# Performance work log

Measured on AMD Instinct MI355X. Metric: run time of the kernel, lower is better.

Reference implementation:

```python
import jax, jax.numpy as jnp
import numpy as np

B, T, N, F, H, K = 16, 24, 1329, 130, 15, 5


def setup_inputs() -> dict:
    key = jax.random.key(0)
    ks = jax.random.split(key, 14)
    var1 = 2.0 / (N + F)
    var2 = 2.0 / (F + 1)
    return {
        "seq": jax.random.uniform(ks[0], (B, T, N), jnp.float32),
        "A_hat": jax.random.uniform(ks[1], (N, N), jnp.float32) / N,  # normalized-adjacency scale
        "weight": jax.random.normal(ks[2], (N, F), jnp.float32) * var1,
        "bias": jax.random.normal(ks[3], (F,), jnp.float32) * var1,
        "weight2": jax.random.normal(ks[4], (F, 1), jnp.float32) * var2,
        "bias2": jax.random.normal(ks[5], (1,), jnp.float32) * var2,
        "W_ih": jax.random.normal(ks[6], (4 * H, N), jnp.float32) * 0.05,
        "W_hh": jax.random.normal(ks[7], (4 * H, H), jnp.float32) * 0.05,
        "b_ih": jax.random.normal(ks[8], (4 * H,), jnp.float32) * 0.05,
        "b_hh": jax.random.normal(ks[9], (4 * H,), jnp.float32) * 0.05,
        "h0": jax.random.normal(ks[10], (B, H), jnp.float32),
        "c0": jax.random.normal(ks[11], (B, H), jnp.float32),
        "fc_w": jax.random.normal(ks[12], (K, N, H), jnp.float32) * 0.05,
        "fc_b": jax.random.normal(ks[13], (K, N), jnp.float32) * 0.05,
    }


def reference(seq, A_hat, weight, bias, weight2, bias2,
              W_ih, W_hh, b_ih, b_hh, h0, c0, fc_w, fc_b):
    # --- GCN part (vectorized over all batch/timestep pairs) ---
    # diag(seq[b,t]) @ weight == row-scale of weight by seq values
    X = seq[..., None] * weight + bias                       # [B,T,N,F]
    X = jax.nn.relu(jnp.einsum('mn,btnf->btmf', A_hat, X))   # [B,T,N,F]
    Y = jnp.einsum('btnf,fo->btno', X, weight2)[..., 0] + bias2  # [B,T,N]
    Y = jax.nn.relu(jnp.einsum('mn,btn->btm', A_hat, Y))     # [B,T,N]

    # --- LSTM (PyTorch gate order i, f, g, o) ---
    def step(carry, x_t):
        h, c = carry
        g = x_t @ W_ih.T + h @ W_hh.T + b_ih + b_hh          # [B,4H]
        i, f, gg, o = jnp.split(g, 4, axis=-1)
        c = jax.nn.sigmoid(f) * c + jax.nn.sigmoid(i) * jnp.tanh(gg)
        h = jax.nn.sigmoid(o) * jnp.tanh(c)
        return (h, c), None

    (h_last, _), _ = jax.lax.scan(step, (h0, c0), jnp.swapaxes(Y, 0, 1))

    # --- 5 FC heads on sigmoid(last hidden) ---
    s = jax.nn.sigmoid(h_last)                               # [B,H]
    outs = jnp.tanh(jnp.einsum('koh,bh->kbo', fc_w, s) + fc_b[:, None, :])  # [K,B,N]
    return tuple(outs[k] for k in range(K))
```

## Files before the change

kernel.cpp:

```cpp
#include <hip/hip_runtime.h>
#include <hip/hip_bf16.h>
#include <math.h>

#define NN 1329
#define FF 130
#define BB 16
#define TT 24
#define HH 15
#define KK 5
#define BT (BB*TT)
#define G4 (4*HH)

#define KPAD 1344
#define NKC 42
#define MFRAG 88
#define NMT 11
#define NCF 9
#define NBTF 24
#define ZSPLIT 7

typedef __attribute__((ext_vector_type(8))) short short8v;
typedef __attribute__((ext_vector_type(4))) float f32x4;

#define OFS_ROWSUM 0
#define OFS_SPAD   1408
#define OFS_Y1     (OFS_SPAD + BT*KPAD)
#define OFS_Y2P    (OFS_Y1 + BT*NN)
#define OFS_WIHT   (OFS_Y2P + ZSPLIT*BT*NN)
#define OFS_XW     (OFS_WIHT + NN*64)
#define OFS_S      (OFS_XW + BT*64)
#define OFS_END_F  (OFS_S + 256)
#define ABF_ELEMS  (NKC*MFRAG*64*8)
#define WBF_ELEMS  (NKC*NCF*64*8)
#define Y1BF_ELEMS (NKC*NBTF*64*8)

__device__ __forceinline__ float sigmoidf(float x) { return 1.f / (1.f + expf(-x)); }

__device__ __forceinline__ unsigned short bf16rne(float x) {
    unsigned u = __float_as_uint(x);
    return (unsigned short)((u + 0x7fffu + ((u >> 16) & 1u)) >> 16);
}
__device__ __forceinline__ float bf16lo(unsigned a) { return __uint_as_float(a << 16); }
__device__ __forceinline__ float bf16hi(unsigned a) { return __uint_as_float(a & 0xffff0000u); }
__device__ __forceinline__ unsigned cvtpk2(float lo, float hi) {
    unsigned r;
    asm volatile("v_cvt_pk_bf16_f32 %0, %1, %2" : "=v"(r) : "v"(lo), "v"(hi));
    return r;
}

__device__ __forceinline__ void gll16(const void* g, void* l) {
    __builtin_amdgcn_global_load_lds((const __attribute__((address_space(1))) unsigned*)g,
                                     (__attribute__((address_space(3))) unsigned*)l, 16, 0, 0);
}

#define NB_APREP 924
#define NB_WPREP 95
#define NB_SPREP 2016
#define NB_WIHT  333
#define NB_ROWS  NN
#define NB_PREP  (NB_APREP+NB_WPREP+NB_SPREP+NB_WIHT+NB_ROWS)

__global__ __launch_bounds__(256) void k_prep(
    const float* __restrict__ A, const float* __restrict__ W,
    const float* __restrict__ seq, const float* __restrict__ Wih,
    unsigned short* __restrict__ Abf, unsigned short* __restrict__ Wbf,
    float* __restrict__ spad, float* __restrict__ WihT, float* __restrict__ rowsum)
{
    __shared__ float r4[4];
    const int bid = blockIdx.x;
    const int tid = threadIdx.x;
    if (bid < NB_APREP) {
        int s = bid*256 + tid;
        int l = s & 63;
        int t = s >> 6;
        int mf = t % MFRAG;
        int kcg = t / MFRAG;
        int m = mf*16 + (l & 15);
        int kb = kcg*32 + (l >> 4)*8;
        union { uint4 u4; unsigned short us[8]; } ow;
#pragma unroll
        for (int j = 0; j < 8; j++) {
            int k = kb + j;
            float x = (m < NN && k < NN) ? A[(size_t)m*NN + k] : 0.f;
            ow.us[j] = bf16rne(x);
        }
        *(uint4*)(Abf + (size_t)s*8) = ow.u4;
    } else if (bid < NB_APREP+NB_WPREP) {
        int s = (bid-NB_APREP)*256 + tid;
        if (s < NKC*NCF*64) {
            int l = s & 63;
            int t = s >> 6;
            int cf = t % NCF;
            int kcg = t / NCF;
            int f = cf*16 + (l & 15);
            int kb = kcg*32 + (l >> 4)*8;
            union { uint4 u4; unsigned short us[8]; } ow;
#pragma unroll
            for (int j = 0; j < 8; j++) {
                int k = kb + j;
                float x = (k < NN && f < FF) ? W[(size_t)k*FF + f] : 0.f;
                ow.us[j] = bf16rne(x);
            }
            *(uint4*)(Wbf + (size_t)s*8) = ow.u4;
        }
    } else if (bid < NB_APREP+NB_WPREP+NB_SPREP) {
        int idx = (bid-NB_APREP-NB_WPREP)*256 + tid;
        int bt = idx / KPAD;
        int k  = idx - bt*KPAD;
        spad[idx] = (k < NN) ? seq[(size_t)bt*NN + k] : 0.f;
    } else if (bid < NB_APREP+NB_WPREP+NB_SPREP+NB_WIHT) {
        int idx = (bid-NB_APREP-NB_WPREP-NB_SPREP)*256 + tid;
        if (idx < NN*64) {
            int n = idx >> 6;
            int g = idx & 63;
            WihT[idx] = (g < G4) ? Wih[(size_t)g*NN + n] : 0.f;
        }
    } else {
        int m = bid - (NB_APREP+NB_WPREP+NB_SPREP+NB_WIHT);
        float a = 0.f;
        for (int n = tid; n < NN; n += 256) a += A[(size_t)m*NN + n];
#pragma unroll
        for (int off = 32; off; off >>= 1) a += __shfl_down(a, off, 64);
        if ((tid & 63) == 0) r4[tid >> 6] = a;
        __syncthreads();
        if (tid == 0) rowsum[m] = r4[0]+r4[1]+r4[2]+r4[3];
    }
}

__global__ __launch_bounds__(256,2) void k_gcn1(
    const unsigned short* __restrict__ Abf, const unsigned short* __restrict__ Wbf,
    const float* __restrict__ spad,
    const float* __restrict__ bias, const float* __restrict__ w2, const float* __restrict__ bias2,
    const float* __restrict__ rowsum, float* __restrict__ Y1)
{
    __shared__ __align__(16) short Blds[2][NCF*64*8];

    const int id = blockIdx.x;
    const int mt = id / BT;
    const int bt = id - mt*BT;
    const int m0 = mt*128;
    const int tid = threadIdx.x;
    const int lane = tid & 63;
    const int wv = tid >> 6;
    const float* sb = spad + (size_t)bt*KPAD;
    const int klane = (lane >> 4)*8;

    f32x4 acc[2][NCF];
#pragma unroll
    for (int rf = 0; rf < 2; rf++)
#pragma unroll
        for (int cf = 0; cf < NCF; cf++) acc[rf][cf] = (f32x4){0.f, 0.f, 0.f, 0.f};

    auto stageB = [&](int kcg, int nb) {
        const unsigned short* wsrc = Wbf + (size_t)kcg*(NCF*64*8);
#pragma unroll
        for (int it = 0; it < 2; ++it) {
            int slot = it*256 + tid;
            gll16(wsrc + (size_t)slot*8, &Blds[nb][slot*8]);
        }
        if (tid < 64) {
            int slot = 512 + tid;
            gll16(wsrc + (size_t)slot*8, &Blds[nb][slot*8]);
        }
    };
    uint4 r0, r1; float4 s0, s1;
    auto loadA = [&](int kcg) {
        const unsigned short* p = Abf + ((size_t)(kcg*MFRAG + mt*8 + 2*wv)*64 + lane)*8;
        r0 = *(const uint4*)p;
        r1 = *(const uint4*)(p + 64*8);
        const float* sp = sb + kcg*32 + klane;
        s0 = *(const float4*)sp;
        s1 = *(const float4*)(sp + 4);
    };
    auto scaleA = [&](uint4 r) -> short8v {
        union { uint4 u4; short8v s8; } o;
        o.u4.x = cvtpk2(bf16lo(r.x)*s0.x, bf16hi(r.x)*s0.y);
        o.u4.y = cvtpk2(bf16lo(r.y)*s0.z, bf16hi(r.y)*s0.w);
        o.u4.z = cvtpk2(bf16lo(r.z)*s1.x, bf16hi(r.z)*s1.y);
        o.u4.w = cvtpk2(bf16lo(r.w)*s1.z, bf16hi(r.w)*s1.w);
        return o.s8;
    };

    stageB(0, 0);
    loadA(0);
    __syncthreads();
    short8v a0 = scaleA(r0), a1 = scaleA(r1);

    for (int t = 0; t < NKC; ++t) {
        const int cur = t & 1;
        if (t + 1 < NKC) { stageB(t+1, cur^1); loadA(t+1); }
        short8v bfr[NCF];
#pragma unroll
        for (int cf = 0; cf < NCF; cf++)
            bfr[cf] = *(const short8v*)&Blds[cur][(cf*64 + lane)*8];
#pragma unroll
        for (int cf = 0; cf < NCF; cf++) {
            acc[0][cf] = __builtin_amdgcn_mfma_f32_16x16x32_bf16(a0, bfr[cf], acc[0][cf], 0, 0, 0);
            acc[1][cf] = __builtin_amdgcn_mfma_f32_16x16x32_bf16(a1, bfr[cf], acc[1][cf], 0, 0, 0);
        }
        if (t + 1 < NKC) { a0 = scaleA(r0); a1 = scaleA(r1); }
        __syncthreads();
    }

    const int fcol = lane & 15;
    const int rgrp = lane >> 4;
    float bv[NCF], wv2[NCF];
#pragma unroll
    for (int cf = 0; cf < NCF; cf++) {
        int f = cf*16 + fcol;
        bv[cf]  = (f < FF) ? bias[f] : 0.f;
        wv2[cf] = (f < FF) ? w2[f]   : 0.f;
    }
    float b2 = bias2[0];
#pragma unroll
    for (int rf = 0; rf < 2; rf++) {
#pragma unroll
        for (int r = 0; r < 4; r++) {
            int m = m0 + (2*wv + rf)*16 + rgrp*4 + r;
            float rs = (m < NN) ? rowsum[m] : 0.f;
            float p = 0.f;
#pragma unroll
            for (int cf = 0; cf < NCF; cf++)
                p += fmaxf(acc[rf][cf][r] + bv[cf]*rs, 0.f) * wv2[cf];
            p += __shfl_xor(p, 1, 64);
            p += __shfl_xor(p, 2, 64);
            p += __shfl_xor(p, 4, 64);
            p += __shfl_xor(p, 8, 64);
            if (fcol == 0 && m < NN) Y1[(size_t)bt*NN + m] = p + b2;
        }
    }
}

__global__ __launch_bounds__(256) void k_y1bf(const float* __restrict__ Y1, unsigned short* __restrict__ Y1bf) {
    int s = blockIdx.x*256 + threadIdx.x;
    int l = s & 63;
    int t = s >> 6;
    int btf = t % NBTF;
    int kcg = t / NBTF;
    int bt = btf*16 + (l & 15);
    int nb = kcg*32 + (l >> 4)*8;
    const float* yp = Y1 + (size_t)bt*NN;
    union { uint4 u4; unsigned short us[8]; } ow;
#pragma unroll
    for (int j = 0; j < 8; j++) {
        int n = nb + j;
        ow.us[j] = bf16rne((n < NN) ? yp[n] : 0.f);
    }
    *(uint4*)(Y1bf + (size_t)s*8) = ow.u4;
}

__global__ __launch_bounds__(256) void k_gcn2(
    const unsigned short* __restrict__ Abf, const unsigned short* __restrict__ Y1bf,
    float* __restrict__ Y2p)
{
    const int mt = blockIdx.x;
    const int btg = blockIdx.y;
    const int z = blockIdx.z;
    const int tid = threadIdx.x;
    const int lane = tid & 63;
    const int wv = tid >> 6;

    f32x4 acc[2][4];
#pragma unroll
    for (int rf = 0; rf < 2; rf++)
#pragma unroll
        for (int cf = 0; cf < 4; cf++) acc[rf][cf] = (f32x4){0.f, 0.f, 0.f, 0.f};

#pragma unroll
    for (int kk = 0; kk < 6; ++kk) {
        int kcg = z*6 + kk;
        const unsigned short* ap = Abf + ((size_t)(kcg*MFRAG + mt*8 + 2*wv)*64 + lane)*8;
        short8v a0 = *(const short8v*)ap;
        short8v a1 = *(const short8v*)(ap + 64*8);
#pragma unroll
        for (int cf = 0; cf < 4; cf++) {
            const unsigned short* bp = Y1bf + ((size_t)((kcg*NBTF + btg*4 + cf)*64) + lane)*8;
            short8v b = *(const short8v*)bp;
            acc[0][cf] = __builtin_amdgcn_mfma_f32_16x16x32_bf16(a0, b, acc[0][cf], 0, 0, 0);
            acc[1][cf] = __builtin_amdgcn_mfma_f32_16x16x32_bf16(a1, b, acc[1][cf], 0, 0, 0);
        }
    }
#pragma unroll
    for (int rf = 0; rf < 2; rf++)
#pragma unroll
        for (int cf = 0; cf < 4; cf++)
#pragma unroll
            for (int r = 0; r < 4; r++) {
                int m = mt*128 + (2*wv + rf)*16 + (lane >> 4)*4 + r;
                int btv = btg*64 + cf*16 + (lane & 15);
                if (m < NN) Y2p[((size_t)z*NN + m)*BT + btv] = acc[rf][cf][r];
            }
}

__global__ __launch_bounds__(256) void k_xw(const float* __restrict__ Y2p,
    const float* __restrict__ WihT, float* __restrict__ xW)
{
    __shared__ float red[4][64];
    int bt = blockIdx.x;
    int tid = threadIdx.x;
    int p = tid >> 6, g = tid & 63;
    float acc = 0.f;
    int nend = min((p+1)*336, NN);
    for (int n = p*336; n < nend; ++n) {
        float y = 0.f;
#pragma unroll
        for (int z = 0; z < ZSPLIT; ++z)
            y += Y2p[((size_t)z*NN + n)*BT + bt];
        y = fmaxf(y, 0.f);
        acc = fmaf(y, WihT[n*64 + g], acc);
    }
    red[p][g] = acc;
    __syncthreads();
    if (tid < 64) {
        float v = red[0][tid] + red[1][tid] + red[2][tid] + red[3][tid];
        if (tid < G4) xW[bt*64 + tid] = v;
    }
}

__global__ __launch_bounds__(64) void k_lstm(const float* __restrict__ xW,
    const float* __restrict__ Whh, const float* __restrict__ bih, const float* __restrict__ bhh,
    const float* __restrict__ h0, const float* __restrict__ c0, float* __restrict__ s_out)
{
    __shared__ float h_s[16];
    int b = blockIdx.x;
    int lane = threadIdx.x;
    float whh_r[HH];
    float bs = 0.f;
    if (lane < G4) {
        bs = bih[lane] + bhh[lane];
#pragma unroll
        for (int k = 0; k < HH; k++) whh_r[k] = Whh[lane*HH + k];
    }
    float c_r = 0.f, h_last = 0.f;
    if (lane < HH) { h_s[lane] = h0[b*HH + lane]; c_r = c0[b*HH + lane]; }
    __syncthreads();
    for (int t = 0; t < TT; ++t) {
        float v = 0.f;
        if (lane < G4) {
            v = xW[(size_t)(b*TT + t)*64 + lane] + bs;
#pragma unroll
            for (int k = 0; k < HH; k++) v = fmaf(whh_r[k], h_s[k], v);
        }
        float vi = __shfl(v, lane, 64);
        float vf = __shfl(v, HH   + lane, 64);
        float vg = __shfl(v, 2*HH + lane, 64);
        float vo = __shfl(v, 3*HH + lane, 64);
        __syncthreads();
        if (lane < HH) {
            float c = sigmoidf(vf)*c_r + sigmoidf(vi)*tanhf(vg);
            c_r = c;
            float h = sigmoidf(vo)*tanhf(c);
            h_s[lane] = h;
            h_last = h;
        }
        __syncthreads();
    }
    if (lane < HH) s_out[b*HH + lane] = sigmoidf(h_last);
}

__global__ __launch_bounds__(256) void k_heads(const float* __restrict__ fc_w,
    const float* __restrict__ fc_b, const float* __restrict__ s, float* __restrict__ out)
{
    __shared__ float s_s[BB*HH];
    int tid = threadIdx.x;
    if (tid < BB*HH) s_s[tid] = s[tid];
    __syncthreads();
    int idx = blockIdx.x*256 + tid;
    if (idx >= KK*BB*NN) return;
    int k = idx / (BB*NN);
    int rem = idx - k*(BB*NN);
    int b = rem / NN;
    int n = rem - b*NN;
    const float* wp = fc_w + ((size_t)k*NN + n)*HH;
    const float* sp = s_s + b*HH;
    float v = fc_b[k*NN + n];
#pragma unroll
    for (int h = 0; h < HH; h++) v = fmaf(wp[h], sp[h], v);
    out[idx] = tanhf(v);
}

extern "C" void kernel_launch(void* const* d_in, const int* in_sizes, int n_in,
                              void* d_out, int out_size, void* d_ws, size_t ws_size,
                              hipStream_t stream) {
    const float* seq   = (const float*)d_in[0];
    const float* A     = (const float*)d_in[1];
    const float* W     = (const float*)d_in[2];
    const float* bias  = (const float*)d_in[3];
    const float* w2    = (const float*)d_in[4];
    const float* bias2 = (const float*)d_in[5];
    const float* Wih   = (const float*)d_in[6];
    const float* Whh   = (const float*)d_in[7];
    const float* bih   = (const float*)d_in[8];
    const float* bhh   = (const float*)d_in[9];
    const float* h0    = (const float*)d_in[10];
    const float* c0    = (const float*)d_in[11];
    const float* fcw   = (const float*)d_in[12];
    const float* fcb   = (const float*)d_in[13];
    float* ws = (float*)d_ws;
    float* rowsum = ws + OFS_ROWSUM;
    float* spad   = ws + OFS_SPAD;
    float* Y1     = ws + OFS_Y1;
    float* Y2p    = ws + OFS_Y2P;
    float* WihT   = ws + OFS_WIHT;
    float* xW     = ws + OFS_XW;
    float* s_sig  = ws + OFS_S;
    unsigned short* Abf  = (unsigned short*)(ws + OFS_END_F);
    unsigned short* Wbf  = Abf + ABF_ELEMS;
    unsigned short* Y1bf = Wbf + WBF_ELEMS;
    float* out = (float*)d_out;

    hipLaunchKernelGGL(k_prep, dim3(NB_PREP), dim3(256), 0, stream,
                       A, W, seq, Wih, Abf, Wbf, spad, WihT, rowsum);
    hipLaunchKernelGGL(k_gcn1, dim3(NMT*BT), dim3(256), 0, stream,
                       Abf, Wbf, spad, bias, w2, bias2, rowsum, Y1);
    hipLaunchKernelGGL(k_y1bf, dim3(NKC*NBTF*64/256), dim3(256), 0, stream, Y1, Y1bf);
    hipLaunchKernelGGL(k_gcn2, dim3(NMT, 6, ZSPLIT), dim3(256), 0, stream, Abf, Y1bf, Y2p);
    hipLaunchKernelGGL(k_xw, dim3(BT), dim3(256), 0, stream, Y2p, WihT, xW);
    hipLaunchKernelGGL(k_lstm, dim3(BB), dim3(64), 0, stream, xW, Whh, bih, bhh, h0, c0, s_sig);
    hipLaunchKernelGGL(k_heads, dim3((KK*BB*NN + 255)/256), dim3(256), 0, stream, fcw, fcb, s_sig, out);
}
```

Measured before the change: 451.8 us.

## Fuse Y1 bf16 conversion into gcn2 and do input projection with MFMA

Removes the separate k_y1bf conversion kernel: gcn2 now reads fp32 Y1 directly and packs it to bf16 in registers. gcn2 no longer splits K into seven partial sums. It runs the full K loop per block, applies ReLU, and writes bf16 output already laid out as MFMA A-fragments. The scalar k_xw reduction is replaced by k_xwm, which multiplies those fragments by a bf16 pre-swizzled W_ih on the matrix units. This cuts the partial-sum traffic, two kernel launches and the fp32 dot-product loop. In exchange, gcn2 has far fewer blocks with a longer serial K loop, and the LSTM input is quantised to bf16.

```diff
diff --git a/kernel.cpp b/kernel.cpp
--- a/kernel.cpp
+++ b/kernel.cpp
@@ -17,7 +17,7 @@
 #define NMT 11
 #define NCF 9
 #define NBTF 24
-#define ZSPLIT 7
+#define NKCO 44
 
 typedef __attribute__((ext_vector_type(8))) short short8v;
 typedef __attribute__((ext_vector_type(4))) float f32x4;
@@ -25,14 +25,13 @@
 #define OFS_ROWSUM 0
 #define OFS_SPAD   1408
 #define OFS_Y1     (OFS_SPAD + BT*KPAD)
-#define OFS_Y2P    (OFS_Y1 + BT*NN)
-#define OFS_WIHT   (OFS_Y2P + ZSPLIT*BT*NN)
-#define OFS_XW     (OFS_WIHT + NN*64)
+#define OFS_XW     (OFS_Y1 + BT*NN)
 #define OFS_S      (OFS_XW + BT*64)
 #define OFS_END_F  (OFS_S + 256)
 #define ABF_ELEMS  (NKC*MFRAG*64*8)
 #define WBF_ELEMS  (NKC*NCF*64*8)
-#define Y1BF_ELEMS (NKC*NBTF*64*8)
+#define WTB_ELEMS  (NKC*4*64*8)
+#define Y2A_ELEMS  (NKCO*NBTF*64*8)
 
 __device__ __forceinline__ float sigmoidf(float x) { return 1.f / (1.f + expf(-x)); }
 
@@ -56,15 +55,15 @@
 #define NB_APREP 924
 #define NB_WPREP 95
 #define NB_SPREP 2016
-#define NB_WIHT  333
+#define NB_WTB   42
 #define NB_ROWS  NN
-#define NB_PREP  (NB_APREP+NB_WPREP+NB_SPREP+NB_WIHT+NB_ROWS)
+#define NB_PREP  (NB_APREP+NB_WPREP+NB_SPREP+NB_WTB+NB_ROWS)
 
 __global__ __launch_bounds__(256) void k_prep(
     const float* __restrict__ A, const float* __restrict__ W,
     const float* __restrict__ seq, const float* __restrict__ Wih,
     unsigned short* __restrict__ Abf, unsigned short* __restrict__ Wbf,
-    float* __restrict__ spad, float* __restrict__ WihT, float* __restrict__ rowsum)
+    float* __restrict__ spad, unsigned short* __restrict__ WihTbf, float* __restrict__ rowsum)
 {
     __shared__ float r4[4];
     const int bid = blockIdx.x;
@@ -108,15 +107,24 @@
         int bt = idx / KPAD;
         int k  = idx - bt*KPAD;
         spad[idx] = (k < NN) ? seq[(size_t)bt*NN + k] : 0.f;
-    } else if (bid < NB_APREP+NB_WPREP+NB_SPREP+NB_WIHT) {
-        int idx = (bid-NB_APREP-NB_WPREP-NB_SPREP)*256 + tid;
-        if (idx < NN*64) {
-            int n = idx >> 6;
-            int g = idx & 63;
-            WihT[idx] = (g < G4) ? Wih[(size_t)g*NN + n] : 0.f;
-        }
+    } else if (bid < NB_APREP+NB_WPREP+NB_SPREP+NB_WTB) {
+        int s = (bid-NB_APREP-NB_WPREP-NB_SPREP)*256 + tid;
+        int l = s & 63;
+        int t = s >> 6;
+        int gf = t & 3;
+        int kcg = t >> 2;
+        int g = gf*16 + (l & 15);
+        int nb = kcg*32 + (l >> 4)*8;
+        union { uint4 u4; unsigned short us[8]; } ow;
+#pragma unroll
+        for (int j = 0; j < 8; j++) {
+            int n = nb + j;
+            float x = (g < G4 && n < NN) ? Wih[(size_t)g*NN + n] : 0.f;
+            ow.us[j] = bf16rne(x);
+        }
+        *(uint4*)(WihTbf + (size_t)s*8) = ow.u4;
     } else {
-        int m = bid - (NB_APREP+NB_WPREP+NB_SPREP+NB_WIHT);
+        int m = bid - (NB_APREP+NB_WPREP+NB_SPREP+NB_WTB);
         float a = 0.f;
         for (int n = tid; n < NN; n += 256) a += A[(size_t)m*NN + n];
 #pragma unroll
@@ -231,90 +239,102 @@
     }
 }
 
-__global__ __launch_bounds__(256) void k_y1bf(const float* __restrict__ Y1, unsigned short* __restrict__ Y1bf) {
-    int s = blockIdx.x*256 + threadIdx.x;
-    int l = s & 63;
-    int t = s >> 6;
-    int btf = t % NBTF;
-    int kcg = t / NBTF;
-    int bt = btf*16 + (l & 15);
-    int nb = kcg*32 + (l >> 4)*8;
-    const float* yp = Y1 + (size_t)bt*NN;
-    union { uint4 u4; unsigned short us[8]; } ow;
-#pragma unroll
-    for (int j = 0; j < 8; j++) {
-        int n = nb + j;
-        ow.us[j] = bf16rne((n < NN) ? yp[n] : 0.f);
-    }
-    *(uint4*)(Y1bf + (size_t)s*8) = ow.u4;
-}
-
 __global__ __launch_bounds__(256) void k_gcn2(
-    const unsigned short* __restrict__ Abf, const unsigned short* __restrict__ Y1bf,
-    float* __restrict__ Y2p)
-{
-    const int mt = blockIdx.x;
+    const unsigned short* __restrict__ Abf, const float* __restrict__ Y1,
+    unsigned short* __restrict__ Y2A)
+{
+    const int mt  = blockIdx.x;
     const int btg = blockIdx.y;
-    const int z = blockIdx.z;
     const int tid = threadIdx.x;
     const int lane = tid & 63;
     const int wv = tid >> 6;
-
-    f32x4 acc[2][4];
+    const int q = lane >> 4;
+
+    f32x4 acc[2][2];
 #pragma unroll
     for (int rf = 0; rf < 2; rf++)
 #pragma unroll
-        for (int cf = 0; cf < 4; cf++) acc[rf][cf] = (f32x4){0.f, 0.f, 0.f, 0.f};
-
-#pragma unroll
-    for (int kk = 0; kk < 6; ++kk) {
-        int kcg = z*6 + kk;
+        for (int cf = 0; cf < 2; cf++) acc[rf][cf] = (f32x4){0.f, 0.f, 0.f, 0.f};
+
+    const float* y1r0 = Y1 + (size_t)((btg*2 + 0)*16 + (lane & 15))*NN;
+    const float* y1r1 = Y1 + (size_t)((btg*2 + 1)*16 + (lane & 15))*NN;
+    const int nq = q*8;
+
+    for (int kcg = 0; kcg < NKC; ++kcg) {
         const unsigned short* ap = Abf + ((size_t)(kcg*MFRAG + mt*8 + 2*wv)*64 + lane)*8;
         short8v a0 = *(const short8v*)ap;
         short8v a1 = *(const short8v*)(ap + 64*8);
-#pragma unroll
-        for (int cf = 0; cf < 4; cf++) {
-            const unsigned short* bp = Y1bf + ((size_t)((kcg*NBTF + btg*4 + cf)*64) + lane)*8;
-            short8v b = *(const short8v*)bp;
-            acc[0][cf] = __builtin_amdgcn_mfma_f32_16x16x32_bf16(a0, b, acc[0][cf], 0, 0, 0);
-            acc[1][cf] = __builtin_amdgcn_mfma_f32_16x16x32_bf16(a1, b, acc[1][cf], 0, 0, 0);
-        }
-    }
-#pragma unroll
-    for (int rf = 0; rf < 2; rf++)
-#pragma unroll
-        for (int cf = 0; cf < 4; cf++)
-#pragma unroll
-            for (int r = 0; r < 4; r++) {
-                int m = mt*128 + (2*wv + rf)*16 + (lane >> 4)*4 + r;
-                int btv = btg*64 + cf*16 + (lane & 15);
-                if (m < NN) Y2p[((size_t)z*NN + m)*BT + btv] = acc[rf][cf][r];
+        int n0 = kcg*32 + nq;
+        union { uint4 u4; short8v s8; } b0, b1;
+        if (kcg < NKC-1) {
+            float4 x0 = *(const float4*)(y1r0 + n0);
+            float4 x1 = *(const float4*)(y1r0 + n0 + 4);
+            b0.u4.x = cvtpk2(x0.x, x0.y); b0.u4.y = cvtpk2(x0.z, x0.w);
+            b0.u4.z = cvtpk2(x1.x, x1.y); b0.u4.w = cvtpk2(x1.z, x1.w);
+            float4 y0 = *(const float4*)(y1r1 + n0);
+            float4 y1v = *(const float4*)(y1r1 + n0 + 4);
+            b1.u4.x = cvtpk2(y0.x, y0.y); b1.u4.y = cvtpk2(y0.z, y0.w);
+            b1.u4.z = cvtpk2(y1v.x, y1v.y); b1.u4.w = cvtpk2(y1v.z, y1v.w);
+        } else {
+            float xa[8], xb[8];
+#pragma unroll
+            for (int j = 0; j < 8; j++) {
+                int n = n0 + j;
+                xa[j] = (n < NN) ? y1r0[n] : 0.f;
+                xb[j] = (n < NN) ? y1r1[n] : 0.f;
             }
-}
-
-__global__ __launch_bounds__(256) void k_xw(const float* __restrict__ Y2p,
-    const float* __restrict__ WihT, float* __restrict__ xW)
-{
-    __shared__ float red[4][64];
-    int bt = blockIdx.x;
-    int tid = threadIdx.x;
-    int p = tid >> 6, g = tid & 63;
-    float acc = 0.f;
-    int nend = min((p+1)*336, NN);
-    for (int n = p*336; n < nend; ++n) {
-        float y = 0.f;
-#pragma unroll
-        for (int z = 0; z < ZSPLIT; ++z)
-            y += Y2p[((size_t)z*NN + n)*BT + bt];
-        y = fmaxf(y, 0.f);
-        acc = fmaf(y, WihT[n*64 + g], acc);
-    }
-    red[p][g] = acc;
-    __syncthreads();
-    if (tid < 64) {
-        float v = red[0][tid] + red[1][tid] + red[2][tid] + red[3][tid];
-        if (tid < G4) xW[bt*64 + tid] = v;
-    }
+            b0.u4.x = cvtpk2(xa[0], xa[1]); b0.u4.y = cvtpk2(xa[2], xa[3]);
+            b0.u4.z = cvtpk2(xa[4], xa[5]); b0.u4.w = cvtpk2(xa[6], xa[7]);
+            b1.u4.x = cvtpk2(xb[0], xb[1]); b1.u4.y = cvtpk2(xb[2], xb[3]);
+            b1.u4.z = cvtpk2(xb[4], xb[5]); b1.u4.w = cvtpk2(xb[6], xb[7]);
+        }
+        acc[0][0] = __builtin_amdgcn_mfma_f32_16x16x32_bf16(a0, b0.s8, acc[0][0], 0, 0, 0);
+        acc[1][0] = __builtin_amdgcn_mfma_f32_16x16x32_bf16(a1, b0.s8, acc[1][0], 0, 0, 0);
+        acc[0][1] = __builtin_amdgcn_mfma_f32_16x16x32_bf16(a0, b1.s8, acc[0][1], 0, 0, 0);
+        acc[1][1] = __builtin_amdgcn_mfma_f32_16x16x32_bf16(a1, b1.s8, acc[1][1], 0, 0, 0);
+    }
+
+    const int kcgo = mt*4 + wv;
+    const int jofs = (q & 1)*4;
+#pragma unroll
+    for (int rf = 0; rf < 2; rf++) {
+        int lp = (rf*2 + (q >> 1))*16 + (lane & 15);
+#pragma unroll
+        for (int cf = 0; cf < 2; cf++) {
+            int btf = btg*2 + cf;
+            uint2 w2v;
+            w2v.x = cvtpk2(fmaxf(acc[rf][cf][0], 0.f), fmaxf(acc[rf][cf][1], 0.f));
+            w2v.y = cvtpk2(fmaxf(acc[rf][cf][2], 0.f), fmaxf(acc[rf][cf][3], 0.f));
+            *(uint2*)(Y2A + ((size_t)(kcgo*NBTF + btf)*64 + lp)*8 + jofs) = w2v;
+        }
+    }
+}
+
+__global__ __launch_bounds__(64) void k_xwm(
+    const unsigned short* __restrict__ Y2A, const unsigned short* __restrict__ WihTbf,
+    float* __restrict__ xW)
+{
+    const int btf = blockIdx.x;
+    const int lane = threadIdx.x;
+    f32x4 acc[4];
+#pragma unroll
+    for (int gf = 0; gf < 4; gf++) acc[gf] = (f32x4){0.f, 0.f, 0.f, 0.f};
+
+    for (int kcg = 0; kcg < NKC; ++kcg) {
+        short8v a = *(const short8v*)(Y2A + ((size_t)(kcg*NBTF + btf)*64 + lane)*8);
+#pragma unroll
+        for (int gf = 0; gf < 4; gf++) {
+            short8v b = *(const short8v*)(WihTbf + ((size_t)(kcg*4 + gf)*64 + lane)*8);
+            acc[gf] = __builtin_amdgcn_mfma_f32_16x16x32_bf16(a, b, acc[gf], 0, 0, 0);
+        }
+    }
+#pragma unroll
+    for (int gf = 0; gf < 4; gf++)
+#pragma unroll
+        for (int r = 0; r < 4; r++) {
+            int bt = btf*16 + (lane >> 4)*4 + r;
+            xW[(size_t)bt*64 + gf*16 + (lane & 15)] = acc[gf][r];
+        }
 }
 
 __global__ __launch_bounds__(64) void k_lstm(const float* __restrict__ xW,
@@ -400,22 +420,20 @@
     float* rowsum = ws + OFS_ROWSUM;
     float* spad   = ws + OFS_SPAD;
     float* Y1     = ws + OFS_Y1;
-    float* Y2p    = ws + OFS_Y2P;
-    float* WihT   = ws + OFS_WIHT;
     float* xW     = ws + OFS_XW;
     float* s_sig  = ws + OFS_S;
-    unsigned short* Abf  = (unsigned short*)(ws + OFS_END_F);
-    unsigned short* Wbf  = Abf + ABF_ELEMS;
-    unsigned short* Y1bf = Wbf + WBF_ELEMS;
+    unsigned short* Abf    = (unsigned short*)(ws + OFS_END_F);
+    unsigned short* Wbf    = Abf + ABF_ELEMS;
+    unsigned short* WihTbf = Wbf + WBF_ELEMS;
+    unsigned short* Y2A    = WihTbf + WTB_ELEMS;
     float* out = (float*)d_out;
 
     hipLaunchKernelGGL(k_prep, dim3(NB_PREP), dim3(256), 0, stream,
-                       A, W, seq, Wih, Abf, Wbf, spad, WihT, rowsum);
+                       A, W, seq, Wih, Abf, Wbf, spad, WihTbf, rowsum);
     hipLaunchKernelGGL(k_gcn1, dim3(NMT*BT), dim3(256), 0, stream,
                        Abf, Wbf, spad, bias, w2, bias2, rowsum, Y1);
-    hipLaunchKernelGGL(k_y1bf, dim3(NKC*NBTF*64/256), dim3(256), 0, stream, Y1, Y1bf);
-    hipLaunchKernelGGL(k_gcn2, dim3(NMT, 6, ZSPLIT), dim3(256), 0, stream, Abf, Y1bf, Y2p);
-    hipLaunchKernelGGL(k_xw, dim3(BT), dim3(256), 0, stream, Y2p, WihT, xW);
+    hipLaunchKernelGGL(k_gcn2, dim3(NMT, 12), dim3(256), 0, stream, Abf, Y1, Y2A);
+    hipLaunchKernelGGL(k_xwm, dim3(NBTF), dim3(64), 0, stream, Y2A, WihTbf, xW);
     hipLaunchKernelGGL(k_lstm, dim3(BB), dim3(64), 0, stream, xW, Whh, bih, bhh, h0, c0, s_sig);
     hipLaunchKernelGGL(k_heads, dim3((KK*BB*NN + 255)/256), dim3(256), 0, stream, fcw, fcb, s_sig, out);
 }
```

Result: faster. 367.6 us (-18.6%).
